# Optimization experiments

Hardware: AMD Instinct MI355X
Metric: run time of the kernel (lower is better)

Reference implementation:

```python
import jax, jax.numpy as jnp
import numpy as np

BN_EPS = 1e-5


def setup_inputs() -> dict:
    key = jax.random.key(0)
    ks = jax.random.split(key, 12)
    B, N, d_e, d_a = 16, 2048, 256, 64
    s_e = 1.0 / np.sqrt(d_e)
    return {
        "x":    jax.random.normal(ks[0], (B, N, d_e), dtype=jnp.float32),
        "Wq":   jax.random.uniform(ks[1], (d_e, d_a), jnp.float32, -s_e, s_e),
        "bq":   jax.random.uniform(ks[2], (d_a,), jnp.float32, -s_e, s_e),
        "Wk":   jax.random.uniform(ks[3], (d_e, d_a), jnp.float32, -s_e, s_e),
        "bk":   jax.random.uniform(ks[4], (d_a,), jnp.float32, -s_e, s_e),
        "Wv":   jax.random.uniform(ks[5], (d_e, d_e), jnp.float32, -s_e, s_e),
        "bv":   jax.random.uniform(ks[6], (d_e,), jnp.float32, -s_e, s_e),
        "Wl":   jax.random.uniform(ks[7], (d_e, d_e), jnp.float32, -s_e, s_e),
        "bl":   jax.random.uniform(ks[8], (d_e,), jnp.float32, -s_e, s_e),
        "gamma": jnp.ones((d_e,), jnp.float32),
        "beta":  jnp.zeros((d_e,), jnp.float32),
    }


def reference(x, Wq, bq, Wk, bk, Wv, bv, Wl, bl, gamma, beta):
    # x: [B, N, d_e]
    q = x @ Wq + bq          # [B, N, d_a]
    k = x @ Wk + bk          # [B, N, d_a]
    v = x @ Wv + bv          # [B, N, d_e]
    d_a = q.shape[-1]
    # NOTE: PCT scales by d_a, not sqrt(d_a) -- faithful to the source.
    score = jnp.einsum('bnd,bmd->bnm', q, k) / jnp.asarray(d_a, q.dtype)
    score = jax.nn.softmax(score, axis=2)          # [B, N, N]
    attn = jnp.einsum('bnm,bmd->bnd', score, v)    # [B, N, d_e]
    # LBR: linear + BatchNorm1d (training-mode batch stats over B,N) + ReLU
    h = attn @ Wl + bl                             # [B, N, d_e]
    mean = jnp.mean(h, axis=(0, 1))
    var = jnp.mean((h - mean) ** 2, axis=(0, 1))   # biased variance (torch BN)
    y = jax.nn.relu((h - mean) * jax.lax.rsqrt(var + BN_EPS) * gamma + beta)
    return y + x
```

## Files before the change

kernel.cpp:

```cpp
#include <hip/hip_runtime.h>
#include <hip/hip_bf16.h>

#define B_  16
#define N_  2048
#define DE  256
#define DA  64
#define T_  (B_*N_)

typedef __attribute__((ext_vector_type(4)))  float f32x4;
typedef __attribute__((ext_vector_type(8)))  short bf16x8;
typedef unsigned short u16;

__device__ __forceinline__ float bf2f(u16 x){
  unsigned v = ((unsigned)x) << 16;
  return __builtin_bit_cast(float, v);
}
__device__ __forceinline__ u16 f2bf(float f){
  unsigned u = __builtin_bit_cast(unsigned, f);
  u += 0x7fffu + ((u >> 16) & 1u);
  return (u16)(u >> 16);
}
__device__ __forceinline__ f32x4 mfma16(bf16x8 a, bf16x8 b, f32x4 c){
  return __builtin_amdgcn_mfma_f32_16x16x32_bf16(a, b, c, 0, 0, 0);
}
__device__ __forceinline__ bool is_f32(const void* gsig){
  return *(const unsigned*)gsig == 0x3F800000u;
}
__device__ __forceinline__ float gload(const void* p, long i, bool f32m){
  return f32m ? ((const float*)p)[i] : bf2f(((const u16*)p)[i]);
}

__global__ void k_prep(const void* __restrict__ Wq, const void* __restrict__ Wk,
                       const void* __restrict__ Wv, const void* __restrict__ Wl,
                       const void* __restrict__ bq, const void* __restrict__ bk,
                       const void* __restrict__ bv, const void* __restrict__ bl,
                       const void* __restrict__ gsig,
                       u16* __restrict__ Wt, u16* __restrict__ Wlt,
                       float* __restrict__ bqkv, float* __restrict__ blf){
  bool f32m = is_f32(gsig);
  int i = blockIdx.x*256 + threadIdx.x;
  if (i < 384*256){
    int n = i/256, kk = i%256;
    float v;
    if (n < 64)       v = gload(Wq, (long)kk*64 + n, f32m);
    else if (n < 128) v = gload(Wk, (long)kk*64 + (n-64), f32m);
    else              v = gload(Wv, (long)kk*256 + (n-128), f32m);
    Wt[i] = f2bf(v);
  }
  int j = i - 384*256;
  if (j >= 0 && j < 256*256){
    int n = j/256, kk = j%256;
    Wlt[j] = f2bf(gload(Wl, (long)kk*256 + n, f32m));
  }
  int m = i - (384*256 + 256*256);
  if (m >= 0 && m < 384){
    float v;
    if (m < 64)       v = gload(bq, m, f32m);
    else if (m < 128) v = gload(bk, m-64, f32m);
    else              v = gload(bv, m-128, f32m);
    bqkv[m] = v;
  }
  int p = i - (384*256 + 256*256 + 384);
  if (p >= 0 && p < 256) blf[p] = gload(bl, p, f32m);
}

__global__ __launch_bounds__(256) void k_qkv(
    const void* __restrict__ xg, const void* __restrict__ gsig,
    const u16* __restrict__ Wt, const float* __restrict__ bqkv,
    u16* __restrict__ qo, u16* __restrict__ ko, u16* __restrict__ vtt){
  __shared__ __align__(16) u16 sm[256*72];
  bool f32m = is_f32(gsig);
  int tid = threadIdx.x, lane = tid & 63, w = tid >> 6;
  int lm = lane & 15, lq = lane >> 4;
  long t0 = (long)blockIdx.x * 64;

  #pragma unroll
  for(int it=0; it<8; it++){
    int c = tid + 256*it;
    int tok = c >> 5, kk = (c & 31)*8;
    bf16x8 d;
    if (f32m){
      const float* xf = (const float*)xg + (t0+tok)*DE + kk;
      f32x4 a = *(const f32x4*)xf;
      f32x4 b2 = *(const f32x4*)(xf+4);
      #pragma unroll
      for(int j2=0;j2<4;j2++){ d[j2]=(short)f2bf(a[j2]); d[4+j2]=(short)f2bf(b2[j2]); }
    } else {
      d = *(const bf16x8*)((const u16*)xg + (t0+tok)*DE + kk);
    }
    *(bf16x8*)(sm + tok*264 + kk) = d;
  }
  __syncthreads();

  f32x4 acc[4][6];
  #pragma unroll
  for(int mt=0;mt<4;mt++)
    #pragma unroll
    for(int nt=0;nt<6;nt++){ acc[mt][nt][0]=0.f;acc[mt][nt][1]=0.f;acc[mt][nt][2]=0.f;acc[mt][nt][3]=0.f; }

  for(int s=0;s<8;s++){
    int kk = s*32 + lq*8;
    bf16x8 afr[4];
    #pragma unroll
    for(int mt=0;mt<4;mt++)
      afr[mt] = *(const bf16x8*)(sm + (mt*16+lm)*264 + kk);
    #pragma unroll
    for(int nt=0;nt<6;nt++){
      int col = w*96 + nt*16 + lm;
      bf16x8 bfr = *(const bf16x8*)(Wt + (long)col*DE + kk);
      #pragma unroll
      for(int mt=0;mt<4;mt++)
        acc[mt][nt] = mfma16(afr[mt], bfr, acc[mt][nt]);
    }
  }
  __syncthreads();

  #pragma unroll
  for(int nt=0;nt<6;nt++){
    int col = w*96 + nt*16 + lm;
    float bias = bqkv[col];
    #pragma unroll
    for(int mt=0;mt<4;mt++){
      #pragma unroll
      for(int r=0;r<4;r++){
        int tokin = mt*16 + lq*4 + r;
        u16 o = f2bf(acc[mt][nt][r] + bias);
        if (col < 64)        qo[(t0+tokin)*DA + col]      = o;
        else if (col < 128)  ko[(t0+tokin)*DA + (col-64)] = o;
        else                 sm[(col-128)*72 + tokin]     = o;
      }
    }
  }
  __syncthreads();
  int b = (int)(t0 >> 11), kt = (int)((t0 & 2047) >> 6);
  u16* tile = vtt + (long)(b*32 + kt)*16384;
  #pragma unroll
  for(int g=0; g<8; g++){
    bf16x8 d = *(const bf16x8*)(sm + tid*72 + g*8);
    *(bf16x8*)(tile + tid*64 + g*8) = d;
  }
}

__global__ __launch_bounds__(256, 2) void k_attn(
    const u16* __restrict__ qg, const u16* __restrict__ kg,
    const u16* __restrict__ vtt, u16* __restrict__ attng){
  __shared__ __align__(16) u16 P[2][64*72];
  __shared__ float lred[4][64];

  int bid = blockIdx.x;
  int b  = 2*(bid & 7) + ((bid >> 3) >> 5);
  int qb = (bid >> 3) & 31;
  int tid = threadIdx.x, lane = tid & 63, w = tid >> 6;
  int lm = lane & 15, lq = lane >> 4;

  long kb0 = (long)b * N_;
  long rb  = kb0 + qb*64;

  const float cexp = 0.0225421850f;

  const u16* qbase = qg + rb*DA;
  bf16x8 qf[4][2];
  #pragma unroll
  for(int rt=0;rt<4;rt++)
    #pragma unroll
    for(int s=0;s<2;s++)
      qf[rt][s] = *(const bf16x8*)(qbase + (long)(rt*16+lm)*DA + s*32 + lq*8);

  f32x4 o[4][4];
  #pragma unroll
  for(int rt=0;rt<4;rt++)
    #pragma unroll
    for(int nt=0;nt<4;nt++){ o[rt][nt][0]=0.f;o[rt][nt][1]=0.f;o[rt][nt][2]=0.f;o[rt][nt][3]=0.f; }
  float ls[4][4];
  #pragma unroll
  for(int rt=0;rt<4;rt++)
    #pragma unroll
    for(int r=0;r<4;r++) ls[rt][r] = 0.f;

  const u16* kptr = kg  + (kb0 + 16*w + lm)*DA + lq*8;
  const u16* vptr = vtt + (long)b*524288 + (64*w + lm)*64 + lq*8;

  #define LDS_BARRIER asm volatile("s_waitcnt lgkmcnt(0)\n\ts_barrier" ::: "memory")

  {
    bf16x8 k0 = *(const bf16x8*)(kptr);
    bf16x8 k1 = *(const bf16x8*)(kptr + 32);
    #pragma unroll
    for(int rt=0;rt<4;rt++){
      f32x4 a4; a4[0]=0.f;a4[1]=0.f;a4[2]=0.f;a4[3]=0.f;
      a4 = mfma16(qf[rt][0], k0, a4);
      a4 = mfma16(qf[rt][1], k1, a4);
      #pragma unroll
      for(int r=0;r<4;r++){
        float e = exp2f(a4[r] * cexp);
        ls[rt][r] += e;
        P[0][(rt*16 + lq*4 + r)*72 + 16*w + lm] = f2bf(e);
      }
    }
  }
  LDS_BARRIER;

  for(int t=1; t<N_/64; t++){
    const u16* Pr = P[(t-1)&1];
    u16*       Pw = P[t&1];
    bf16x8 pf[4][2];
    #pragma unroll
    for(int rt=0;rt<4;rt++){
      pf[rt][0] = *(const bf16x8*)(Pr + (rt*16+lm)*72 + lq*8);
      pf[rt][1] = *(const bf16x8*)(Pr + (rt*16+lm)*72 + 32 + lq*8);
    }
    const u16* kr_ = kptr + (long)t*64*DA;
    bf16x8 k0 = *(const bf16x8*)(kr_);
    bf16x8 k1 = *(const bf16x8*)(kr_ + 32);
    const u16* vn = vptr + (long)(t-1)*16384;
    bf16x8 vr[4][2];
    #pragma unroll
    for(int nt=0;nt<4;nt++){
      vr[nt][0] = *(const bf16x8*)(vn + nt*1024);
      vr[nt][1] = *(const bf16x8*)(vn + nt*1024 + 32);
    }
    f32x4 S[4];
    #pragma unroll
    for(int rt=0;rt<4;rt++){
      f32x4 a4; a4[0]=0.f;a4[1]=0.f;a4[2]=0.f;a4[3]=0.f;
      a4 = mfma16(qf[rt][0], k0, a4);
      a4 = mfma16(qf[rt][1], k1, a4);
      S[rt] = a4;
    }
    #pragma unroll
    for(int rt=0;rt<4;rt++)
      #pragma unroll
      for(int nt=0;nt<4;nt++){
        o[rt][nt] = mfma16(pf[rt][0], vr[nt][0], o[rt][nt]);
        o[rt][nt] = mfma16(pf[rt][1], vr[nt][1], o[rt][nt]);
      }
    #pragma unroll
    for(int rt=0;rt<4;rt++)
      #pragma unroll
      for(int r=0;r<4;r++){
        float e = exp2f(S[rt][r] * cexp);
        ls[rt][r] += e;
        Pw[(rt*16 + lq*4 + r)*72 + 16*w + lm] = f2bf(e);
      }
    LDS_BARRIER;
  }

  {
    const u16* Pr = P[(N_/64 - 1)&1];
    bf16x8 pf[4][2];
    #pragma unroll
    for(int rt=0;rt<4;rt++){
      pf[rt][0] = *(const bf16x8*)(Pr + (rt*16+lm)*72 + lq*8);
      pf[rt][1] = *(const bf16x8*)(Pr + (rt*16+lm)*72 + 32 + lq*8);
    }
    const u16* vn = vptr + (long)(N_/64 - 1)*16384;
    #pragma unroll
    for(int nt=0;nt<4;nt++){
      bf16x8 v0 = *(const bf16x8*)(vn + nt*1024);
      bf16x8 v1 = *(const bf16x8*)(vn + nt*1024 + 32);
      #pragma unroll
      for(int rt=0;rt<4;rt++){
        o[rt][nt] = mfma16(pf[rt][0], v0, o[rt][nt]);
        o[rt][nt] = mfma16(pf[rt][1], v1, o[rt][nt]);
      }
    }
  }
  #undef LDS_BARRIER

  #pragma unroll
  for(int rt=0;rt<4;rt++)
    #pragma unroll
    for(int r=0;r<4;r++){
      float s = ls[rt][r];
      s += __shfl_xor(s, 1, 64);
      s += __shfl_xor(s, 2, 64);
      s += __shfl_xor(s, 4, 64);
      s += __shfl_xor(s, 8, 64);
      ls[rt][r] = s;
    }
  if (lm == 0){
    #pragma unroll
    for(int rt=0;rt<4;rt++)
      #pragma unroll
      for(int r=0;r<4;r++)
        lred[w][rt*16 + lq*4 + r] = ls[rt][r];
  }
  __syncthreads();
  u16* abase = attng + rb*DE + 64*w;
  #pragma unroll
  for(int rt=0;rt<4;rt++){
    #pragma unroll
    for(int r=0;r<4;r++){
      int row = rt*16 + lq*4 + r;
      float inv = 1.0f / (lred[0][row] + lred[1][row] + lred[2][row] + lred[3][row]);
      #pragma unroll
      for(int nt=0;nt<4;nt++)
        abase[(long)row*DE + nt*16 + lm] = f2bf(o[rt][nt][r] * inv);
    }
  }
}

__global__ __launch_bounds__(256) void k_hgemm(
    const u16* __restrict__ attng, const u16* __restrict__ Wlt,
    const float* __restrict__ blf, u16* __restrict__ hg, float* __restrict__ stats){
  __shared__ __align__(16) u16 xs[64*264];
  int tid = threadIdx.x, lane = tid & 63, w = tid >> 6;
  int lm = lane & 15, lq = lane >> 4;
  long t0 = (long)blockIdx.x * 64;

  const u16* src = attng + t0*DE;
  #pragma unroll
  for(int i=0;i<8;i++){
    int c16 = tid + 256*i;
    int tok = c16 >> 5, kk = (c16 & 31)*8;
    *(bf16x8*)(xs + tok*264 + kk) = *(const bf16x8*)(src + (long)tok*DE + kk);
  }
  __syncthreads();

  f32x4 acc[4][4];
  #pragma unroll
  for(int mt=0;mt<4;mt++)
    #pragma unroll
    for(int nt=0;nt<4;nt++){ acc[mt][nt][0]=0.f;acc[mt][nt][1]=0.f;acc[mt][nt][2]=0.f;acc[mt][nt][3]=0.f; }

  for(int s=0;s<8;s++){
    int kk = s*32 + lq*8;
    bf16x8 afr[4];
    #pragma unroll
    for(int mt=0;mt<4;mt++)
      afr[mt] = *(const bf16x8*)(xs + (mt*16+lm)*264 + kk);
    #pragma unroll
    for(int nt=0;nt<4;nt++){
      int col = w*64 + nt*16 + lm;
      bf16x8 bfr = *(const bf16x8*)(Wlt + (long)col*DE + kk);
      #pragma unroll
      for(int mt=0;mt<4;mt++)
        acc[mt][nt] = mfma16(afr[mt], bfr, acc[mt][nt]);
    }
  }
  #pragma unroll
  for(int nt=0;nt<4;nt++){
    int col = w*64 + nt*16 + lm;
    float bias = blf[col];
    float s1 = 0.f, s2 = 0.f;
    #pragma unroll
    for(int mt=0;mt<4;mt++){
      #pragma unroll
      for(int r=0;r<4;r++){
        long tok = t0 + mt*16 + lq*4 + r;
        float val = acc[mt][nt][r] + bias;
        hg[tok*DE + col] = f2bf(val);
        s1 += val; s2 += val*val;
      }
    }
    s1 += __shfl_xor(s1, 16, 64); s2 += __shfl_xor(s2, 16, 64);
    s1 += __shfl_xor(s1, 32, 64); s2 += __shfl_xor(s2, 32, 64);
    if (lq == 0){
      atomicAdd(&stats[col], s1);
      atomicAdd(&stats[256 + col], s2);
    }
  }
}

__global__ __launch_bounds__(256) void k_apply(
    const u16* __restrict__ hg, const void* __restrict__ xg,
    const void* __restrict__ gamma, const void* __restrict__ beta,
    const float* __restrict__ stats, void* __restrict__ outg){
  __shared__ float sc[256], sh[256];
  bool f32m = is_f32(gamma);
  int tid = threadIdx.x;
  {
    const float inv_n = 1.0f/32768.0f;
    float mean = stats[tid]*inv_n;
    float var  = stats[256+tid]*inv_n - mean*mean;
    float s = gload(gamma, tid, f32m) * rsqrtf(var + 1e-5f);
    sc[tid] = s;
    sh[tid] = gload(beta, tid, f32m) - mean*s;
  }
  __syncthreads();

  long i = (long)blockIdx.x*256 + tid;
  long base = i*8;
  int ch0 = (int)(base & 255);
  bf16x8 hv = *(const bf16x8*)(hg + base);
  float xv[8];
  if (f32m){
    f32x4 a = *((const f32x4*)xg + i*2);
    f32x4 b2 = *((const f32x4*)xg + i*2 + 1);
    #pragma unroll
    for(int j=0;j<4;j++){ xv[j]=a[j]; xv[4+j]=b2[j]; }
  } else {
    bf16x8 xb = *((const bf16x8*)xg + i);
    #pragma unroll
    for(int j=0;j<8;j++) xv[j] = bf2f((u16)xb[j]);
  }
  float y[8];
  #pragma unroll
  for(int j=0;j<8;j++){
    float h = bf2f((u16)hv[j]);
    y[j] = fmaxf(h*sc[ch0+j] + sh[ch0+j], 0.f) + xv[j];
  }
  if (f32m){
    f32x4 o0, o1;
    #pragma unroll
    for(int j=0;j<4;j++){ o0[j]=y[j]; o1[j]=y[4+j]; }
    *((f32x4*)outg + i*2) = o0;
    *((f32x4*)outg + i*2 + 1) = o1;
  } else {
    bf16x8 ov;
    #pragma unroll
    for(int j=0;j<8;j++) ov[j] = (short)f2bf(y[j]);
    *((bf16x8*)outg + i) = ov;
  }
}

extern "C" void kernel_launch(void* const* d_in, const int* in_sizes, int n_in,
                              void* d_out, int out_size, void* d_ws, size_t ws_size,
                              hipStream_t stream){
  const void* x     = d_in[0];
  const void* Wq    = d_in[1];
  const void* bq    = d_in[2];
  const void* Wk    = d_in[3];
  const void* bk    = d_in[4];
  const void* Wv    = d_in[5];
  const void* bv    = d_in[6];
  const void* Wl    = d_in[7];
  const void* bl    = d_in[8];
  const void* gamma = d_in[9];
  const void* beta  = d_in[10];

  char* ws = (char*)d_ws;
  u16*   Wt    = (u16*)  (ws + 0x0);
  u16*   Wlt   = (u16*)  (ws + 0x30000);
  float* bqkv  = (float*)(ws + 0x50000);
  float* blf   = (float*)(ws + 0x50600);
  float* stats = (float*)(ws + 0x50A00);
  u16*   qw    = (u16*)  (ws + 0x60000);
  u16*   kw    = (u16*)  (ws + 0x460000);
  u16*   vtt   = (u16*)  (ws + 0x860000);
  u16*   attnw = (u16*)  (ws + 0x1860000);
  u16*   hw    = (u16*)  (ws + 0x2860000);

  hipMemsetAsync(stats, 0, 512*sizeof(float), stream);
  k_prep  <<<643, 256, 0, stream>>>(Wq, Wk, Wv, Wl, bq, bk, bv, bl, gamma, Wt, Wlt, bqkv, blf);
  k_qkv   <<<512, 256, 0, stream>>>(x, gamma, Wt, bqkv, qw, kw, vtt);
  k_attn  <<<512, 256, 0, stream>>>(qw, kw, vtt, attnw);
  k_hgemm <<<512, 256, 0, stream>>>(attnw, Wlt, blf, hw, stats);
  k_apply <<<4096, 256, 0, stream>>>(hw, x, gamma, beta, stats, d_out);
}
```

Before: 248.7 us.

## Split attention block across eight waves with row-half and column-half work partition

Moves the attention kernel from four to eight waves per block. Each wave now computes scores for one key group and one half of the query rows, and accumulates P·V for a 32-column slice of the output instead of 64. This halves per-wave register state (accumulators, V fragments) and adds waves to hide latency. The cost is that every wave still reads the full P tile from LDS, and the barrier now synchronises twice as many waves.

```diff
diff --git a/kernel.cpp b/kernel.cpp
--- a/kernel.cpp
+++ b/kernel.cpp
@@ -141,7 +141,7 @@
   }
 }
 
-__global__ __launch_bounds__(256, 2) void k_attn(
+__global__ __launch_bounds__(512, 4) void k_attn(
     const u16* __restrict__ qg, const u16* __restrict__ kg,
     const u16* __restrict__ vtt, u16* __restrict__ attng){
   __shared__ __align__(16) u16 P[2][64*72];
@@ -152,6 +152,7 @@
   int qb = (bid >> 3) & 31;
   int tid = threadIdx.x, lane = tid & 63, w = tid >> 6;
   int lm = lane & 15, lq = lane >> 4;
+  int kgi = w & 3, rh = w >> 2;
 
   long kb0 = (long)b * N_;
   long rb  = kb0 + qb*64;
@@ -159,45 +160,46 @@
   const float cexp = 0.0225421850f;
 
   const u16* qbase = qg + rb*DA;
-  bf16x8 qf[4][2];
+  bf16x8 qf[2][2];
+  #pragma unroll
+  for(int rt2=0;rt2<2;rt2++)
+    #pragma unroll
+    for(int s=0;s<2;s++)
+      qf[rt2][s] = *(const bf16x8*)(qbase + (long)(rh*32 + rt2*16 + lm)*DA + s*32 + lq*8);
+
+  f32x4 o[4][2];
   #pragma unroll
   for(int rt=0;rt<4;rt++)
     #pragma unroll
-    for(int s=0;s<2;s++)
-      qf[rt][s] = *(const bf16x8*)(qbase + (long)(rt*16+lm)*DA + s*32 + lq*8);
-
-  f32x4 o[4][4];
-  #pragma unroll
-  for(int rt=0;rt<4;rt++)
-    #pragma unroll
-    for(int nt=0;nt<4;nt++){ o[rt][nt][0]=0.f;o[rt][nt][1]=0.f;o[rt][nt][2]=0.f;o[rt][nt][3]=0.f; }
-  float ls[4][4];
-  #pragma unroll
-  for(int rt=0;rt<4;rt++)
-    #pragma unroll
-    for(int r=0;r<4;r++) ls[rt][r] = 0.f;
-
-  const u16* kptr = kg  + (kb0 + 16*w + lm)*DA + lq*8;
-  const u16* vptr = vtt + (long)b*524288 + (64*w + lm)*64 + lq*8;
+    for(int j=0;j<2;j++){ o[rt][j][0]=0.f;o[rt][j][1]=0.f;o[rt][j][2]=0.f;o[rt][j][3]=0.f; }
+  float ls[2][4];
+  #pragma unroll
+  for(int rt2=0;rt2<2;rt2++)
+    #pragma unroll
+    for(int r=0;r<4;r++) ls[rt2][r] = 0.f;
+
+  const u16* kptr = kg  + (kb0 + kgi*16 + lm)*DA + lq*8;
+  const u16* vptr = vtt + (long)b*524288 + (32*w + lm)*64 + lq*8;
 
   #define LDS_BARRIER asm volatile("s_waitcnt lgkmcnt(0)\n\ts_barrier" ::: "memory")
 
-  {
-    bf16x8 k0 = *(const bf16x8*)(kptr);
-    bf16x8 k1 = *(const bf16x8*)(kptr + 32);
-    #pragma unroll
-    for(int rt=0;rt<4;rt++){
-      f32x4 a4; a4[0]=0.f;a4[1]=0.f;a4[2]=0.f;a4[3]=0.f;
-      a4 = mfma16(qf[rt][0], k0, a4);
-      a4 = mfma16(qf[rt][1], k1, a4);
-      #pragma unroll
-      for(int r=0;r<4;r++){
-        float e = exp2f(a4[r] * cexp);
-        ls[rt][r] += e;
-        P[0][(rt*16 + lq*4 + r)*72 + 16*w + lm] = f2bf(e);
-      }
-    }
-  }
+  #define PHASE_A(t_, PB_) {                                        \
+    const u16* kr_ = kptr + (long)(t_)*64*DA;                       \
+    bf16x8 k0_ = *(const bf16x8*)(kr_);                             \
+    bf16x8 k1_ = *(const bf16x8*)(kr_ + 32);                        \
+    _Pragma("unroll")                                               \
+    for(int rt2=0;rt2<2;rt2++){                                     \
+      f32x4 a4; a4[0]=0.f;a4[1]=0.f;a4[2]=0.f;a4[3]=0.f;            \
+      a4 = mfma16(qf[rt2][0], k0_, a4);                             \
+      a4 = mfma16(qf[rt2][1], k1_, a4);                             \
+      _Pragma("unroll")                                             \
+      for(int r=0;r<4;r++){                                         \
+        float e_ = exp2f(a4[r] * cexp);                             \
+        ls[rt2][r] += e_;                                           \
+        PB_[(rh*32 + rt2*16 + lq*4 + r)*72 + kgi*16 + lm] = f2bf(e_); \
+      } } }
+
+  PHASE_A(0, P[0]);
   LDS_BARRIER;
 
   for(int t=1; t<N_/64; t++){
@@ -209,84 +211,63 @@
       pf[rt][0] = *(const bf16x8*)(Pr + (rt*16+lm)*72 + lq*8);
       pf[rt][1] = *(const bf16x8*)(Pr + (rt*16+lm)*72 + 32 + lq*8);
     }
-    const u16* kr_ = kptr + (long)t*64*DA;
-    bf16x8 k0 = *(const bf16x8*)(kr_);
-    bf16x8 k1 = *(const bf16x8*)(kr_ + 32);
     const u16* vn = vptr + (long)(t-1)*16384;
-    bf16x8 vr[4][2];
-    #pragma unroll
-    for(int nt=0;nt<4;nt++){
-      vr[nt][0] = *(const bf16x8*)(vn + nt*1024);
-      vr[nt][1] = *(const bf16x8*)(vn + nt*1024 + 32);
-    }
-    f32x4 S[4];
-    #pragma unroll
-    for(int rt=0;rt<4;rt++){
-      f32x4 a4; a4[0]=0.f;a4[1]=0.f;a4[2]=0.f;a4[3]=0.f;
-      a4 = mfma16(qf[rt][0], k0, a4);
-      a4 = mfma16(qf[rt][1], k1, a4);
-      S[rt] = a4;
-    }
+    bf16x8 vr[2][2];
+    #pragma unroll
+    for(int j=0;j<2;j++){
+      vr[j][0] = *(const bf16x8*)(vn + j*1024);
+      vr[j][1] = *(const bf16x8*)(vn + j*1024 + 32);
+    }
+    PHASE_A(t, Pw);
     #pragma unroll
     for(int rt=0;rt<4;rt++)
       #pragma unroll
-      for(int nt=0;nt<4;nt++){
-        o[rt][nt] = mfma16(pf[rt][0], vr[nt][0], o[rt][nt]);
-        o[rt][nt] = mfma16(pf[rt][1], vr[nt][1], o[rt][nt]);
-      }
-    #pragma unroll
-    for(int rt=0;rt<4;rt++)
-      #pragma unroll
-      for(int r=0;r<4;r++){
-        float e = exp2f(S[rt][r] * cexp);
-        ls[rt][r] += e;
-        Pw[(rt*16 + lq*4 + r)*72 + 16*w + lm] = f2bf(e);
+      for(int j=0;j<2;j++){
+        o[rt][j] = mfma16(pf[rt][0], vr[j][0], o[rt][j]);
+        o[rt][j] = mfma16(pf[rt][1], vr[j][1], o[rt][j]);
       }
     LDS_BARRIER;
   }
 
   {
     const u16* Pr = P[(N_/64 - 1)&1];
-    bf16x8 pf[4][2];
+    const u16* vn = vptr + (long)(N_/64 - 1)*16384;
     #pragma unroll
     for(int rt=0;rt<4;rt++){
-      pf[rt][0] = *(const bf16x8*)(Pr + (rt*16+lm)*72 + lq*8);
-      pf[rt][1] = *(const bf16x8*)(Pr + (rt*16+lm)*72 + 32 + lq*8);
-    }
-    const u16* vn = vptr + (long)(N_/64 - 1)*16384;
-    #pragma unroll
-    for(int nt=0;nt<4;nt++){
-      bf16x8 v0 = *(const bf16x8*)(vn + nt*1024);
-      bf16x8 v1 = *(const bf16x8*)(vn + nt*1024 + 32);
-      #pragma unroll
-      for(int rt=0;rt<4;rt++){
-        o[rt][nt] = mfma16(pf[rt][0], v0, o[rt][nt]);
-        o[rt][nt] = mfma16(pf[rt][1], v1, o[rt][nt]);
+      bf16x8 pf0 = *(const bf16x8*)(Pr + (rt*16+lm)*72 + lq*8);
+      bf16x8 pf1 = *(const bf16x8*)(Pr + (rt*16+lm)*72 + 32 + lq*8);
+      #pragma unroll
+      for(int j=0;j<2;j++){
+        bf16x8 v0 = *(const bf16x8*)(vn + j*1024);
+        bf16x8 v1 = *(const bf16x8*)(vn + j*1024 + 32);
+        o[rt][j] = mfma16(pf0, v0, o[rt][j]);
+        o[rt][j] = mfma16(pf1, v1, o[rt][j]);
       }
     }
   }
+  #undef PHASE_A
   #undef LDS_BARRIER
 
   #pragma unroll
-  for(int rt=0;rt<4;rt++)
+  for(int rt2=0;rt2<2;rt2++)
     #pragma unroll
     for(int r=0;r<4;r++){
-      float s = ls[rt][r];
+      float s = ls[rt2][r];
       s += __shfl_xor(s, 1, 64);
       s += __shfl_xor(s, 2, 64);
       s += __shfl_xor(s, 4, 64);
       s += __shfl_xor(s, 8, 64);
-      ls[rt][r] = s;
+      ls[rt2][r] = s;
     }
   if (lm == 0){
     #pragma unroll
-    for(int rt=0;rt<4;rt++)
+    for(int rt2=0;rt2<2;rt2++)
       #pragma unroll
       for(int r=0;r<4;r++)
-        lred[w][rt*16 + lq*4 + r] = ls[rt][r];
-  }
-  __syncthreads();
-  u16* abase = attng + rb*DE + 64*w;
+        lred[kgi][rh*32 + rt2*16 + lq*4 + r] = ls[rt2][r];
+  }
+  __syncthreads();
+  u16* abase = attng + rb*DE + 32*w;
   #pragma unroll
   for(int rt=0;rt<4;rt++){
     #pragma unroll
@@ -294,8 +275,8 @@
       int row = rt*16 + lq*4 + r;
       float inv = 1.0f / (lred[0][row] + lred[1][row] + lred[2][row] + lred[3][row]);
       #pragma unroll
-      for(int nt=0;nt<4;nt++)
-        abase[(long)row*DE + nt*16 + lm] = f2bf(o[rt][nt][r] * inv);
+      for(int j=0;j<2;j++)
+        abase[(long)row*DE + j*16 + lm] = f2bf(o[rt][j][r] * inv);
     }
   }
 }
@@ -444,7 +425,7 @@
   hipMemsetAsync(stats, 0, 512*sizeof(float), stream);
   k_prep  <<<643, 256, 0, stream>>>(Wq, Wk, Wv, Wl, bq, bk, bv, bl, gamma, Wt, Wlt, bqkv, blf);
   k_qkv   <<<512, 256, 0, stream>>>(x, gamma, Wt, bqkv, qw, kw, vtt);
-  k_attn  <<<512, 256, 0, stream>>>(qw, kw, vtt, attnw);
+  k_attn  <<<512, 512, 0, stream>>>(qw, kw, vtt, attnw);
   k_hgemm <<<512, 256, 0, stream>>>(attnw, Wlt, blf, hw, stats);
   k_apply <<<4096, 256, 0, stream>>>(hw, x, gamma, beta, stats, d_out);
 }
```

New measurement: 263.6 us. +6.0%, slower.
